# Performance work log

Hardware: AMD Instinct MI355X
Metric: run time of the kernel (lower is better)

The kernel has to match this reference:

```python
import jax, jax.numpy as jnp
import numpy as np

B, K, D_MODEL = 2048, 200, 256
MAX_ATOMS = 13
NUM_BONDS = 5


def setup_inputs() -> dict:
    key = jax.random.key(0)
    ks = jax.random.split(key, 7)
    s1 = 1.0 / np.sqrt(D_MODEL)
    s2 = 1.0 / np.sqrt(K)
    s3 = 1.0 / np.sqrt(2 * MAX_ATOMS)
    return {
        "x": jax.random.normal(ks[0], (B, K, D_MODEL), dtype=jnp.float32),
        "ll1_w": jax.random.uniform(ks[1], (MAX_ATOMS, D_MODEL), jnp.float32, -s1, s1),
        "ll1_b": jax.random.uniform(ks[2], (MAX_ATOMS,), jnp.float32, -s1, s1),
        "ll2_w": jax.random.uniform(ks[3], (MAX_ATOMS, K), jnp.float32, -s2, s2),
        "ll2_b": jax.random.uniform(ks[4], (MAX_ATOMS,), jnp.float32, -s2, s2),
        "fl_w": jax.random.uniform(ks[5], (NUM_BONDS, 2 * MAX_ATOMS), jnp.float32, -s3, s3),
        "fl_b": jax.random.uniform(ks[6], (NUM_BONDS,), jnp.float32, -s3, s3),
        "max_atoms": MAX_ATOMS,
    }


def reference(x, ll1_w, ll1_b, ll2_w, ll2_b, fl_w, fl_b, max_atoms):
    # ll1: (B,K,D) -> (B,K,A); permute -> (B,A,K); ll2: -> (B,A,A)
    e = jnp.einsum('bkd,ad->bka', x, ll1_w) + ll1_b          # (B,K,A)
    r = jnp.einsum('bka,ck->bac', e, ll2_w) + ll2_b          # (B,A,A)
    # final_e[b,i,j,:] = concat(r[b, min(i,j)], r[b, max(i,j)]) -- vectorized
    ii, jj = jnp.meshgrid(jnp.arange(max_atoms), jnp.arange(max_atoms), indexing='ij')
    mn = jnp.minimum(ii, jj)                                 # (A,A)
    mx = jnp.maximum(ii, jj)
    pairs = jnp.concatenate([r[:, mn, :], r[:, mx, :]], axis=-1)  # (B,A,A,2A)
    out = jnp.einsum('bijc,nc->bijn', pairs, fl_w) + fl_b    # (B,A,A,NUM_BONDS)
    return out
```

## Files before the change

### kernel.cpp

```cpp
#include <hip/hip_runtime.h>
#include <cstdint>

#define BB 2048
#define KK 200
#define DD 256
#define AA 13
#define NBOND 5
#define EP 216
#define NBLK (BB / 4)

typedef __attribute__((ext_vector_type(8))) short bf16x8;
typedef __attribute__((ext_vector_type(4))) short bf16x4;
typedef __attribute__((ext_vector_type(4))) float f32x4;

__device__ __forceinline__ short f2bf(float f) {
    unsigned u = __builtin_bit_cast(unsigned, f);
    unsigned r = (u + 0x7fffu + ((u >> 16) & 1u)) >> 16;
    return (short)r;
}

__device__ __forceinline__ bf16x8 cvt8(float4 a, float4 b) {
    bf16x8 f;
    f[0] = f2bf(a.x); f[1] = f2bf(a.y); f[2] = f2bf(a.z); f[3] = f2bf(a.w);
    f[4] = f2bf(b.x); f[5] = f2bf(b.y); f[6] = f2bf(b.z); f[7] = f2bf(b.w);
    return f;
}

__device__ __forceinline__ bf16x4 pack4(f32x4 a) {
    bf16x4 f;
    f[0] = f2bf(a[0]); f[1] = f2bf(a[1]); f[2] = f2bf(a[2]); f[3] = f2bf(a[3]);
    return f;
}

__device__ __forceinline__ bf16x4 pack4f(float4 a) {
    bf16x4 f;
    f[0] = f2bf(a.x); f[1] = f2bf(a.y); f[2] = f2bf(a.z); f[3] = f2bf(a.w);
    return f;
}

__global__ __launch_bounds__(256, 2) void fused(const float* __restrict__ x,
                                                const float* __restrict__ w1,
                                                const float* __restrict__ b1,
                                                const float* __restrict__ w2,
                                                const float* __restrict__ b2,
                                                const float* __restrict__ flw,
                                                const float* __restrict__ flb,
                                                float* __restrict__ out) {
    __shared__ __align__(16) short xs[4][16 * 256];
    __shared__ __align__(16) short eTb[4][16][EP];
    __shared__ float rsw[4][169];

    const int tid  = threadIdx.x;
    const int lane = tid & 63;
    const int wv   = tid >> 6;
    const int col  = lane & 15;
    const int kg   = lane >> 4;
    const long b   = (long)blockIdx.x * 4 + wv;
    const float* xbase = x + b * (size_t)(KK * DD);

    float4 xa[8], xb[8];
    #pragma unroll
    for (int r = 0; r < 8; ++r)
        xa[r] = *(const float4*)(xbase + (size_t)r * DD + lane * 4);
    #pragma unroll
    for (int r = 0; r < 8; ++r)
        xb[r] = *(const float4*)(xbase + (size_t)(8 + r) * DD + lane * 4);

    bf16x8 bfrag[8];
    if (col < AA) {
        const float* wp = w1 + col * DD + kg * 8;
        #pragma unroll
        for (int ks = 0; ks < 8; ++ks)
            bfrag[ks] = cvt8(*(const float4*)(wp + ks * 32),
                             *(const float4*)(wp + ks * 32 + 4));
    } else {
        #pragma unroll
        for (int ks = 0; ks < 8; ++ks) {
            bf16x8 z;
            #pragma unroll
            for (int j = 0; j < 8; ++j) z[j] = 0;
            bfrag[ks] = z;
        }
    }
    const float bias = (col < AA) ? b1[col] : 0.0f;
    const float bc   = (col < AA) ? b2[col] : 0.0f;

    bf16x8 w2f[7];
    #pragma unroll
    for (int ks = 0; ks < 7; ++ks) {
        const int k0 = ks * 32 + kg * 8;
        if (col < AA && k0 < KK) {
            const float* wp = w2 + col * KK + k0;
            w2f[ks] = cvt8(*(const float4*)wp, *(const float4*)(wp + 4));
        } else {
            bf16x8 z;
            #pragma unroll
            for (int j = 0; j < 8; ++j) z[j] = 0;
            w2f[ks] = z;
        }
    }

    for (int i = lane; i < 256; i += 64) {
        eTb[wv][i >> 4][200 + (i & 15)] = 0;
    }
    for (int i = lane; i < 600; i += 64) {
        eTb[wv][13 + i / 200][i % 200] = 0;
    }

    char* xsw = (char*)&xs[wv][0];
    const int wbyte = lane * 8;
    const int rswz  = (col & 7) << 4;

    for (int t = 0; t < 13; ++t) {
        #pragma unroll
        for (int r = 0; r < 8; ++r)
            *(bf16x4*)(xsw + r * 512 + (wbyte ^ ((r & 7) << 4))) = pack4f(xa[r]);
        #pragma unroll
        for (int r = 0; r < 8; ++r) {
            const int rr = 8 + r;
            *(bf16x4*)(xsw + rr * 512 + (wbyte ^ ((rr & 7) << 4))) = pack4f(xb[r]);
        }

        if (t < 12) {
            const int rb = (t + 1) * 16;
            #pragma unroll
            for (int r = 0; r < 8; ++r)
                xa[r] = *(const float4*)(xbase + (size_t)min(rb + r, KK - 1) * DD + lane * 4);
            #pragma unroll
            for (int r = 0; r < 8; ++r)
                xb[r] = *(const float4*)(xbase + (size_t)min(rb + 8 + r, KK - 1) * DD + lane * 4);
        }

        f32x4 acc = {bias, bias, bias, bias};
        #pragma unroll
        for (int s = 0; s < 8; ++s) {
            const bf16x8 afr = *(const bf16x8*)(xsw + col * 512 + ((s * 64 + kg * 16) ^ rswz));
            acc = __builtin_amdgcn_mfma_f32_16x16x32_bf16(afr, bfrag[s], acc, 0, 0, 0);
        }

        if (col < AA) {
            const int row = t * 16 + kg * 4;
            if (row + 3 < KK)
                *(bf16x4*)&eTb[wv][col][row] = pack4(acc);
        }
    }

    f32x4 racc = {0.f, 0.f, 0.f, 0.f};
    #pragma unroll
    for (int ks = 0; ks < 7; ++ks) {
        const bf16x8 afr = *(const bf16x8*)&eTb[wv][col][ks * 32 + kg * 8];
        racc = __builtin_amdgcn_mfma_f32_16x16x32_bf16(afr, w2f[ks], racc, 0, 0, 0);
    }
    if (col < AA) {
        #pragma unroll
        for (int r = 0; r < 4; ++r) {
            const int a = kg * 4 + r;
            if (a < AA) rsw[wv][a * 13 + col] = racc[r] + bc;
        }
    }

    for (int p = lane; p < 169; p += 64) {
        const int i  = p / 13;
        const int j  = p - i * 13;
        const int mn = i < j ? i : j;
        const int mx = i < j ? j : i;
        float o[NBOND];
        #pragma unroll
        for (int n = 0; n < NBOND; ++n) o[n] = flb[n];
        #pragma unroll
        for (int c = 0; c < AA; ++c) {
            const float rm = rsw[wv][mn * 13 + c];
            const float rx = rsw[wv][mx * 13 + c];
            #pragma unroll
            for (int n = 0; n < NBOND; ++n)
                o[n] += rm * flw[n * 26 + c] + rx * flw[n * 26 + 13 + c];
        }
        float* op = out + ((size_t)b * 169 + p) * NBOND;
        #pragma unroll
        for (int n = 0; n < NBOND; ++n) op[n] = o[n];
    }
}

extern "C" void kernel_launch(void* const* d_in, const int* in_sizes, int n_in,
                              void* d_out, int out_size, void* d_ws, size_t ws_size,
                              hipStream_t stream) {
    const float* x   = (const float*)d_in[0];
    const float* w1  = (const float*)d_in[1];
    const float* b1  = (const float*)d_in[2];
    const float* w2  = (const float*)d_in[3];
    const float* b2  = (const float*)d_in[4];
    const float* flw = (const float*)d_in[5];
    const float* flb = (const float*)d_in[6];

    fused<<<NBLK, 256, 0, stream>>>(x, w1, b1, w2, b2, flw, flb, (float*)d_out);
}
```

Measured before the change: 87.49 us.

## Split each molecule's K tiles across two waves sharing LDS intermediate

Each block now handles two molecules, with two waves per molecule: one wave computes K tiles 0-6 and the other tiles 7-12, writing into a shared LDS eT buffer. A block barrier separates this from the second matmul, which both waves compute redundantly. The bond-output loop is split between the two waves. LDS is packed into one buffer to fit three blocks per CU, and the grid doubles. This shortens each wave's serial streaming loop and raises memory-level parallelism, at the cost of a __syncthreads, a redundant second matmul and higher register pressure from the tighter occupancy target. The kernel already streams close to peak HBM bandwidth, which limits how much can be gained.

```diff
diff --git a/kernel.cpp b/kernel.cpp
--- a/kernel.cpp
+++ b/kernel.cpp
@@ -6,12 +6,17 @@
 #define DD 256
 #define AA 13
 #define NBOND 5
-#define EP 216
-#define NBLK (BB / 4)
+#define EP 200
+#define NBLK (BB / 2)
 
 typedef __attribute__((ext_vector_type(8))) short bf16x8;
 typedef __attribute__((ext_vector_type(4))) short bf16x4;
 typedef __attribute__((ext_vector_type(4))) float f32x4;
+
+#define ETB_OFF 0
+#define RSW_OFF 11200
+#define XS_OFF  12560
+#define SMEM_BYTES 45328
 
 __device__ __forceinline__ short f2bf(float f) {
     unsigned u = __builtin_bit_cast(unsigned, f);
@@ -38,7 +43,7 @@
     return f;
 }
 
-__global__ __launch_bounds__(256, 2) void fused(const float* __restrict__ x,
+__global__ __launch_bounds__(256, 3) void fused(const float* __restrict__ x,
                                                 const float* __restrict__ w1,
                                                 const float* __restrict__ b1,
                                                 const float* __restrict__ w2,
@@ -46,25 +51,37 @@
                                                 const float* __restrict__ flw,
                                                 const float* __restrict__ flb,
                                                 float* __restrict__ out) {
-    __shared__ __align__(16) short xs[4][16 * 256];
-    __shared__ __align__(16) short eTb[4][16][EP];
-    __shared__ float rsw[4][169];
+    __shared__ __align__(16) char smem[SMEM_BYTES];
 
     const int tid  = threadIdx.x;
     const int lane = tid & 63;
     const int wv   = tid >> 6;
+    const int mol  = wv >> 1;
+    const int half = wv & 1;
     const int col  = lane & 15;
     const int kg   = lane >> 4;
-    const long b   = (long)blockIdx.x * 4 + wv;
+    const long b   = (long)blockIdx.x * 2 + mol;
     const float* xbase = x + b * (size_t)(KK * DD);
 
+    short* eTb = (short*)(smem + ETB_OFF) + mol * (14 * EP);
+    float* rsw = (float*)(smem + RSW_OFF) + mol * 169;
+    char*  xsw = smem + XS_OFF + wv * (16 * 256 * 2);
+
+    const int T0 = half ? 7 : 0;
+    const int T1 = half ? 13 : 7;
+
+    if (!half && lane < 32) eTb[13 * EP + lane] = 0;
+
     float4 xa[8], xb[8];
-    #pragma unroll
-    for (int r = 0; r < 8; ++r)
-        xa[r] = *(const float4*)(xbase + (size_t)r * DD + lane * 4);
-    #pragma unroll
-    for (int r = 0; r < 8; ++r)
-        xb[r] = *(const float4*)(xbase + (size_t)(8 + r) * DD + lane * 4);
+    {
+        const int rb = T0 * 16;
+        #pragma unroll
+        for (int r = 0; r < 8; ++r)
+            xa[r] = *(const float4*)(xbase + (size_t)min(rb + r, KK - 1) * DD + lane * 4);
+        #pragma unroll
+        for (int r = 0; r < 8; ++r)
+            xb[r] = *(const float4*)(xbase + (size_t)min(rb + 8 + r, KK - 1) * DD + lane * 4);
+    }
 
     bf16x8 bfrag[8];
     if (col < AA) {
@@ -83,7 +100,45 @@
         }
     }
     const float bias = (col < AA) ? b1[col] : 0.0f;
-    const float bc   = (col < AA) ? b2[col] : 0.0f;
+
+    const int wbyte = lane * 8;
+    const int rswz  = (col & 7) << 4;
+
+    for (int t = T0; t < T1; ++t) {
+        #pragma unroll
+        for (int r = 0; r < 8; ++r)
+            *(bf16x4*)(xsw + r * 512 + (wbyte ^ ((r & 7) << 4))) = pack4f(xa[r]);
+        #pragma unroll
+        for (int r = 0; r < 8; ++r) {
+            const int rr = 8 + r;
+            *(bf16x4*)(xsw + rr * 512 + (wbyte ^ ((rr & 7) << 4))) = pack4f(xb[r]);
+        }
+
+        if (t + 1 < T1) {
+            const int rb = (t + 1) * 16;
+            #pragma unroll
+            for (int r = 0; r < 8; ++r)
+                xa[r] = *(const float4*)(xbase + (size_t)min(rb + r, KK - 1) * DD + lane * 4);
+            #pragma unroll
+            for (int r = 0; r < 8; ++r)
+                xb[r] = *(const float4*)(xbase + (size_t)min(rb + 8 + r, KK - 1) * DD + lane * 4);
+        }
+
+        f32x4 acc = {bias, bias, bias, bias};
+        #pragma unroll
+        for (int s = 0; s < 8; ++s) {
+            const bf16x8 afr = *(const bf16x8*)(xsw + col * 512 + ((s * 64 + kg * 16) ^ rswz));
+            acc = __builtin_amdgcn_mfma_f32_16x16x32_bf16(afr, bfrag[s], acc, 0, 0, 0);
+        }
+
+        if (col < AA) {
+            const int row = t * 16 + kg * 4;
+            if (row + 3 < KK)
+                *(bf16x4*)&eTb[col * EP + row] = pack4(acc);
+        }
+    }
+
+    __syncthreads();
 
     bf16x8 w2f[7];
     #pragma unroll
@@ -99,67 +154,24 @@
             w2f[ks] = z;
         }
     }
-
-    for (int i = lane; i < 256; i += 64) {
-        eTb[wv][i >> 4][200 + (i & 15)] = 0;
-    }
-    for (int i = lane; i < 600; i += 64) {
-        eTb[wv][13 + i / 200][i % 200] = 0;
-    }
-
-    char* xsw = (char*)&xs[wv][0];
-    const int wbyte = lane * 8;
-    const int rswz  = (col & 7) << 4;
-
-    for (int t = 0; t < 13; ++t) {
-        #pragma unroll
-        for (int r = 0; r < 8; ++r)
-            *(bf16x4*)(xsw + r * 512 + (wbyte ^ ((r & 7) << 4))) = pack4f(xa[r]);
-        #pragma unroll
-        for (int r = 0; r < 8; ++r) {
-            const int rr = 8 + r;
-            *(bf16x4*)(xsw + rr * 512 + (wbyte ^ ((rr & 7) << 4))) = pack4f(xb[r]);
-        }
-
-        if (t < 12) {
-            const int rb = (t + 1) * 16;
-            #pragma unroll
-            for (int r = 0; r < 8; ++r)
-                xa[r] = *(const float4*)(xbase + (size_t)min(rb + r, KK - 1) * DD + lane * 4);
-            #pragma unroll
-            for (int r = 0; r < 8; ++r)
-                xb[r] = *(const float4*)(xbase + (size_t)min(rb + 8 + r, KK - 1) * DD + lane * 4);
-        }
-
-        f32x4 acc = {bias, bias, bias, bias};
-        #pragma unroll
-        for (int s = 0; s < 8; ++s) {
-            const bf16x8 afr = *(const bf16x8*)(xsw + col * 512 + ((s * 64 + kg * 16) ^ rswz));
-            acc = __builtin_amdgcn_mfma_f32_16x16x32_bf16(afr, bfrag[s], acc, 0, 0, 0);
-        }
-
-        if (col < AA) {
-            const int row = t * 16 + kg * 4;
-            if (row + 3 < KK)
-                *(bf16x4*)&eTb[wv][col][row] = pack4(acc);
-        }
-    }
+    const float bc = (col < AA) ? b2[col] : 0.0f;
 
     f32x4 racc = {0.f, 0.f, 0.f, 0.f};
     #pragma unroll
     for (int ks = 0; ks < 7; ++ks) {
-        const bf16x8 afr = *(const bf16x8*)&eTb[wv][col][ks * 32 + kg * 8];
+        const bf16x8 afr = *(const bf16x8*)&eTb[col * EP + ks * 32 + kg * 8];
         racc = __builtin_amdgcn_mfma_f32_16x16x32_bf16(afr, w2f[ks], racc, 0, 0, 0);
     }
     if (col < AA) {
         #pragma unroll
         for (int r = 0; r < 4; ++r) {
             const int a = kg * 4 + r;
-            if (a < AA) rsw[wv][a * 13 + col] = racc[r] + bc;
-        }
-    }
-
-    for (int p = lane; p < 169; p += 64) {
+            if (a < AA) rsw[a * 13 + col] = racc[r] + bc;
+        }
+    }
+
+    const int pl = half * 64 + lane;
+    for (int p = pl; p < 169; p += 128) {
         const int i  = p / 13;
         const int j  = p - i * 13;
         const int mn = i < j ? i : j;
@@ -169,8 +181,8 @@
         for (int n = 0; n < NBOND; ++n) o[n] = flb[n];
         #pragma unroll
         for (int c = 0; c < AA; ++c) {
-            const float rm = rsw[wv][mn * 13 + c];
-            const float rx = rsw[wv][mx * 13 + c];
+            const float rm = rsw[mn * 13 + c];
+            const float rx = rsw[mx * 13 + c];
             #pragma unroll
             for (int n = 0; n < NBOND; ++n)
                 o[n] += rm * flw[n * 26 + c] + rx * flw[n * 26 + 13 + c];
```

New measurement: 93.20 us. 6.5% more time.
